# Optimization experiments

Hardware: AMD Instinct MI355X
Metric: run time of the kernel (lower is better)

Reference implementation:

```python
import jax, jax.numpy as jnp
import numpy as np

EMBED_DIM = 1024
NUM_HEADS = 16
HEAD_DIM = EMBED_DIM // NUM_HEADS
B, T = 4, 2048


def setup_inputs() -> dict:
    key = jax.random.key(0)
    ks = jax.random.split(key, 5)
    s = 1.0 / np.sqrt(EMBED_DIM)
    x = jax.random.normal(ks[0], (B, T, EMBED_DIM), dtype=jnp.float32)
    W_qkv = jax.random.uniform(ks[1], (EMBED_DIM, 3 * EMBED_DIM), minval=-s, maxval=s, dtype=jnp.float32)
    b_qkv = jax.random.uniform(ks[2], (3 * EMBED_DIM,), minval=-s, maxval=s, dtype=jnp.float32)
    W_proj = jax.random.uniform(ks[3], (EMBED_DIM, EMBED_DIM), minval=-s, maxval=s, dtype=jnp.float32)
    b_proj = jax.random.uniform(ks[4], (EMBED_DIM,), minval=-s, maxval=s, dtype=jnp.float32)
    return {"x": x, "W_qkv": W_qkv, "b_qkv": b_qkv, "W_proj": W_proj, "b_proj": b_proj}


def reference(x, W_qkv, b_qkv, W_proj, b_proj):
    Bq, Tq, C = x.shape
    H, D = NUM_HEADS, HEAD_DIM
    qkv = x @ W_qkv + b_qkv                      # [B,T,3C]
    qkv = qkv.reshape(Bq, Tq, 3, H, D)
    q = qkv[:, :, 0].transpose(0, 2, 1, 3)       # [B,H,T,D]
    k = qkv[:, :, 1].transpose(0, 2, 1, 3)
    v = qkv[:, :, 2].transpose(0, 2, 1, 3)
    scale = 1.0 / jnp.sqrt(jnp.asarray(D, x.dtype))
    attn = jnp.einsum('bhqd,bhkd->bhqk', q, k) * scale  # [B,H,T,T]
    mask = jnp.tril(jnp.ones((Tq, Tq), dtype=bool))     # causal: keep lower triangle
    attn = jnp.where(mask, attn, jnp.asarray(-jnp.inf, attn.dtype))
    attn = jax.nn.softmax(attn, axis=-1)
    out = jnp.einsum('bhqk,bhkd->bhqd', attn, v)        # [B,H,T,D]
    out = out.transpose(0, 2, 1, 3).reshape(Bq, Tq, C)
    return out @ W_proj + b_proj
```

## Files before the change

### kernel.cpp

```cpp
#include <hip/hip_runtime.h>
#include <stdint.h>

typedef unsigned short ushort_t;
typedef __attribute__((ext_vector_type(4))) unsigned int  u32x4;
typedef __attribute__((ext_vector_type(2))) unsigned int  u32x2;
typedef __attribute__((ext_vector_type(4))) float         f32x4;
typedef __attribute__((ext_vector_type(8))) __bf16        bf16x8;

__device__ __forceinline__ ushort_t f2bf(float f) {
    unsigned int u = __float_as_uint(f);
    u += 0x7fffu + ((u >> 16) & 1u);
    return (ushort_t)(u >> 16);
}
__device__ __forceinline__ unsigned int pack2bf(float a, float b) {
    return (unsigned int)f2bf(a) | ((unsigned int)f2bf(b) << 16);
}
__device__ __forceinline__ f32x4 mfma16(bf16x8 a, bf16x8 b, f32x4 c) {
    return __builtin_amdgcn_mfma_f32_16x16x32_bf16(a, b, c, 0, 0, 0);
}
__device__ __forceinline__ bf16x8 ldfrag(const ushort_t* p) {
    return __builtin_bit_cast(bf16x8, *(const u32x4*)p);
}

typedef __attribute__((address_space(3))) unsigned int lds_u32;
typedef __attribute__((address_space(1))) const unsigned int glb_u32;
__device__ __forceinline__ void async16(const void* g, void* l) {
    __builtin_amdgcn_global_load_lds((glb_u32*)g, (lds_u32*)l, 16, 0, 0);
}

#define QSCALE 0.18033688011112042f

__global__ __launch_bounds__(256) void xcast(const float* __restrict__ X,
                                             ushort_t* __restrict__ Xb) {
    long i = ((long)blockIdx.x * 256 + threadIdx.x) * 8;
    float4 a = *(const float4*)(X + i);
    float4 b = *(const float4*)(X + i + 4);
    u32x4 pk;
    pk.x = pack2bf(a.x, a.y); pk.y = pack2bf(a.z, a.w);
    pk.z = pack2bf(b.x, b.y); pk.w = pack2bf(b.z, b.w);
    *(u32x4*)(Xb + i) = pk;
}

__global__ __launch_bounds__(256) void wt_kernel(const float* __restrict__ W,
                                                 ushort_t* __restrict__ Wt,
                                                 int K, int N) {
    __shared__ float tile[32][33];
    int tx = threadIdx.x, ty = threadIdx.y;
    int n0 = blockIdx.x * 32, k0 = blockIdx.y * 32;
    for (int p = 0; p < 4; ++p)
        tile[ty + 8*p][tx] = W[(long)(k0 + ty + 8*p) * N + n0 + tx];
    __syncthreads();
    for (int p = 0; p < 4; ++p)
        Wt[(long)(n0 + ty + 8*p) * K + k0 + tx] = f2bf(tile[tx][ty + 8*p]);
}

__global__ __launch_bounds__(256) void gemm_qkv(const ushort_t* __restrict__ Xb,
                                                const ushort_t* __restrict__ Wt,
                                                const float* __restrict__ bias,
                                                ushort_t* __restrict__ Qo,
                                                ushort_t* __restrict__ Ko,
                                                ushort_t* __restrict__ Vto) {
    __shared__ __align__(16) ushort_t smem[128 * 136];
    ushort_t* As = smem;
    ushort_t* Bs = smem + 128 * 32;

    const int tid  = threadIdx.x;
    const int g    = blockIdx.x;
    const int grp  = g / 192, rr = g % 192;
    const int m0   = (grp * 8 + (rr & 7)) * 128;
    const int n0   = (rr >> 3) * 128;
    const int lane = tid & 63, w = tid >> 6;
    const int quad = lane >> 4, l16 = lane & 15;
    const int wm = (w >> 1) * 64, wn = (w & 1) * 64;

    const int srow = (lane >> 2);
    const int gch  = (lane & 3) ^ ((lane >> 3) & 3);
    const int rslot = (quad ^ ((l16 >> 1) & 3)) * 8;

    f32x4 acc[4][4] = {};

    for (int k0 = 0; k0 < 1024; k0 += 32) {
        __syncthreads();
        for (int c = 0; c < 2; ++c) {
            int chunk = w * 2 + c;
            int row = chunk * 16 + srow;
            async16(&Xb[(long)(m0 + row) * 1024 + k0 + gch * 8], &As[chunk * 512]);
            async16(&Wt[(long)(n0 + row) * 1024 + k0 + gch * 8], &Bs[chunk * 512]);
        }
        __syncthreads();
        bf16x8 af[4], bfr[4];
        for (int i = 0; i < 4; ++i)
            af[i] = ldfrag(&As[(wm + 16*i + l16) * 32 + rslot]);
        for (int j = 0; j < 4; ++j)
            bfr[j] = ldfrag(&Bs[(wn + 16*j + l16) * 32 + rslot]);
        for (int i = 0; i < 4; ++i)
            for (int j = 0; j < 4; ++j)
                acc[i][j] = mfma16(af[i], bfr[j], acc[i][j]);
    }

    float bj[4];
    for (int j = 0; j < 4; ++j) bj[j] = bias[n0 + wn + 16*j + l16];
    const int bb = m0 >> 11, t0m = m0 & 2047;
    __syncthreads();

    if (n0 < 2048) {
        ushort_t* dst = (n0 < 1024) ? Qo : Ko;
        const float scale = (n0 < 1024) ? QSCALE : 1.0f;
        const int nbase = (n0 < 1024) ? n0 : n0 - 1024;
        for (int i = 0; i < 4; ++i)
            for (int j = 0; j < 4; ++j) {
                int nl = wn + 16*j + l16;
                for (int r = 0; r < 4; ++r) {
                    int ml = wm + 16*i + quad*4 + r;
                    smem[ml * 136 + nl] = f2bf((acc[i][j][r] + bj[j]) * scale);
                }
            }
        __syncthreads();
        for (int c = 0; c < 8; ++c) {
            int chunk = tid + 256 * c;
            int row = chunk >> 4, nc = (chunk & 15) * 8;
            int n = nbase + nc;
            int h = n >> 6, d = n & 63;
            *(u32x4*)&dst[((long)(bb*16 + h) * 2048 + t0m + row) * 64 + d] =
                *(const u32x4*)&smem[row * 136 + nc];
        }
    } else {
        for (int i = 0; i < 4; ++i)
            for (int j = 0; j < 4; ++j) {
                int nl = wn + 16*j + l16;
                for (int r = 0; r < 4; ++r) {
                    int ml = wm + 16*i + quad*4 + r;
                    smem[nl * 136 + ml] = f2bf(acc[i][j][r] + bj[j]);
                }
            }
        __syncthreads();
        for (int c = 0; c < 8; ++c) {
            int chunk = tid + 256 * c;
            int row = chunk >> 4, mc = (chunk & 15) * 8;
            int n = n0 - 2048 + row;
            int h = n >> 6, d = n & 63;
            *(u32x4*)&Vto[((long)(bb*16 + h) * 64 + d) * 2048 + t0m + mc] =
                *(const u32x4*)&smem[row * 136 + mc];
        }
    }
}

__global__ __launch_bounds__(256) void attn_kernel(const ushort_t* __restrict__ Q,
                                                   const ushort_t* __restrict__ K,
                                                   const ushort_t* __restrict__ Vt,
                                                   ushort_t* __restrict__ O) {
    __shared__ __align__(16) ushort_t Ks[64 * 64];
    __shared__ __align__(16) ushort_t Vs[64 * 64];
    __shared__ __align__(16) ushort_t Ps[64 * 72];

    const int tid  = threadIdx.x;
    const int lane = tid & 63, w = tid >> 6, quad = lane >> 4, l16 = lane & 15;
    const int p    = blockIdx.x & 15;
    const int bh   = blockIdx.x >> 4;
    const ushort_t* qptr = Q  + (long)bh * 2048 * 64;
    const ushort_t* kptr = K  + (long)bh * 2048 * 64;
    const ushort_t* vptr = Vt + (long)bh * 64 * 2048;
    const int bb2 = bh >> 4, h = bh & 15;

    const int srow = lane >> 3;
    const int gch  = (lane & 7) ^ (lane >> 3);

    for (int ti = 0; ti < 2; ++ti) {
        const int qt = ti ? (31 - p) : p;
        const int qbase = qt * 64;
        const int nkt = qt + 1;

        __syncthreads();
        for (int c = 0; c < 2; ++c) {
            int chunk = tid + 256 * c;
            int row = chunk >> 3, kc = (chunk & 7) * 8;
            *(u32x4*)&Ps[row * 72 + kc] = *(const u32x4*)&qptr[(long)(qbase + row) * 64 + kc];
        }
        __syncthreads();
        bf16x8 qf[2];
        for (int kk = 0; kk < 2; ++kk)
            qf[kk] = ldfrag(&Ps[(16*w + l16) * 72 + kk*32 + quad*8]);

        f32x4 acc[4] = {};
        float l_run = 0.f;

        for (int kt = 0; kt < nkt; ++kt) {
            const int kbase = kt * 64;
            __syncthreads();
            for (int c = 0; c < 2; ++c) {
                int chunk = w * 2 + c;
                int row = chunk * 8 + srow;
                async16(&kptr[(long)(kbase + row) * 64 + gch * 8], &Ks[chunk * 512]);
                async16(&vptr[(long)row * 2048 + kbase + gch * 8], &Vs[chunk * 512]);
            }
            __syncthreads();

            f32x4 s[4] = {};
            for (int kk = 0; kk < 2; ++kk)
                for (int mt = 0; mt < 4; ++mt) {
                    bf16x8 kf = ldfrag(&Ks[(16*mt + l16) * 64 + ((4*kk + quad) ^ (l16 & 7)) * 8]);
                    s[mt] = mfma16(kf, qf[kk], s[mt]);
                }
            if (kt == nkt - 1) {
                int qv = qbase + 16*w + l16;
                for (int mt = 0; mt < 4; ++mt)
                    for (int r = 0; r < 4; ++r)
                        if (kbase + 16*mt + 4*quad + r > qv)
                            s[mt][r] = -__builtin_inff();
            }
            for (int mt = 0; mt < 4; ++mt) {
                float p0 = exp2f(s[mt][0]), p1 = exp2f(s[mt][1]);
                float p2 = exp2f(s[mt][2]), p3 = exp2f(s[mt][3]);
                l_run += (p0 + p1) + (p2 + p3);
                u32x2 pk;
                pk.x = pack2bf(p0, p1);
                pk.y = pack2bf(p2, p3);
                *(u32x2*)&Ps[(16*w + l16) * 72 + 16*mt + 4*quad] = pk;
            }
            for (int kk = 0; kk < 2; ++kk) {
                bf16x8 pf = ldfrag(&Ps[(16*w + l16) * 72 + kk*32 + quad*8]);
                for (int jd = 0; jd < 4; ++jd) {
                    bf16x8 vf = ldfrag(&Vs[(16*jd + l16) * 64 + ((4*kk + quad) ^ (l16 & 7)) * 8]);
                    acc[jd] = mfma16(pf, vf, acc[jd]);
                }
            }
        }

        l_run += __shfl_xor(l_run, 16, 64);
        l_run += __shfl_xor(l_run, 32, 64);
        float linv[4];
        for (int r = 0; r < 4; ++r)
            linv[r] = 1.0f / __shfl(l_run, (lane & 48) | (4*quad + r), 64);
        for (int jd = 0; jd < 4; ++jd)
            for (int r = 0; r < 4; ++r) {
                int t = qbase + 16*w + 4*quad + r;
                int d = 16*jd + l16;
                O[((long)(bb2*2048 + t)) * 1024 + h*64 + d] = f2bf(acc[jd][r] * linv[r]);
            }
    }
}

__global__ __launch_bounds__(256) void gemm_proj(const ushort_t* __restrict__ A,
                                                 const ushort_t* __restrict__ Wt,
                                                 const float* __restrict__ bias,
                                                 float* __restrict__ Out) {
    __shared__ __align__(16) ushort_t As[128 * 32];
    __shared__ __align__(16) ushort_t Bs[128 * 32];

    const int tid  = threadIdx.x;
    const int g    = blockIdx.x;
    const int grp  = g / 64, rr = g % 64;
    const int m0   = (grp * 8 + (rr & 7)) * 128;
    const int n0   = (rr >> 3) * 128;
    const int lane = tid & 63, w = tid >> 6;
    const int quad = lane >> 4, l16 = lane & 15;
    const int wm = (w >> 1) * 64, wn = (w & 1) * 64;

    const int srow = (lane >> 2);
    const int gch  = (lane & 3) ^ ((lane >> 3) & 3);
    const int rslot = (quad ^ ((l16 >> 1) & 3)) * 8;

    f32x4 acc[4][4] = {};

    for (int k0 = 0; k0 < 1024; k0 += 32) {
        __syncthreads();
        for (int c = 0; c < 2; ++c) {
            int chunk = w * 2 + c;
            int row = chunk * 16 + srow;
            async16(&A [(long)(m0 + row) * 1024 + k0 + gch * 8], &As[chunk * 512]);
            async16(&Wt[(long)(n0 + row) * 1024 + k0 + gch * 8], &Bs[chunk * 512]);
        }
        __syncthreads();
        bf16x8 af[4], bfr[4];
        for (int i = 0; i < 4; ++i)
            af[i] = ldfrag(&As[(wm + 16*i + l16) * 32 + rslot]);
        for (int j = 0; j < 4; ++j)
            bfr[j] = ldfrag(&Bs[(wn + 16*j + l16) * 32 + rslot]);
        for (int i = 0; i < 4; ++i)
            for (int j = 0; j < 4; ++j)
                acc[i][j] = mfma16(af[i], bfr[j], acc[i][j]);
    }

    float bj[4];
    for (int j = 0; j < 4; ++j) bj[j] = bias[n0 + wn + 16*j + l16];
    for (int i = 0; i < 4; ++i)
        for (int j = 0; j < 4; ++j)
            for (int r = 0; r < 4; ++r) {
                int m = m0 + wm + 16*i + quad*4 + r;
                int n = n0 + wn + 16*j + l16;
                Out[(long)m * 1024 + n] = acc[i][j][r] + bj[j];
            }
}

extern "C" void kernel_launch(void* const* d_in, const int* in_sizes, int n_in,
                              void* d_out, int out_size, void* d_ws, size_t ws_size,
                              hipStream_t stream) {
    const float* x     = (const float*)d_in[0];
    const float* Wqkv  = (const float*)d_in[1];
    const float* bqkv  = (const float*)d_in[2];
    const float* Wproj = (const float*)d_in[3];
    const float* bproj = (const float*)d_in[4];
    float* out = (float*)d_out;

    ushort_t* wqkvt  = (ushort_t*)d_ws;
    ushort_t* wprojt = wqkvt  + 3072 * 1024;
    ushort_t* Qb     = wprojt + 1024 * 1024;
    ushort_t* Kb     = Qb  + 8388608;
    ushort_t* Vtb    = Kb  + 8388608;
    ushort_t* XbA2   = Vtb + 8388608;

    xcast<<<4096, 256, 0, stream>>>(x, XbA2);
    wt_kernel<<<dim3(96, 32), dim3(32, 8), 0, stream>>>(Wqkv, wqkvt, 1024, 3072);
    wt_kernel<<<dim3(32, 32), dim3(32, 8), 0, stream>>>(Wproj, wprojt, 1024, 1024);
    gemm_qkv<<<1536, 256, 0, stream>>>(XbA2, wqkvt, bqkv, Qb, Kb, Vtb);
    attn_kernel<<<1024, 256, 0, stream>>>(Qb, Kb, Vtb, XbA2);
    gemm_proj<<<512, 256, 0, stream>>>(XbA2, wprojt, bproj, out);
}
```

Measured before the change: 294.3 us.

## Register-prefetch double-buffered GEMMs and attention with 128-row query tiles

Both GEMMs replace the async global-to-LDS loads with register prefetch of the next K slice and double-buffered LDS, so only one barrier is needed per iteration. The attention kernel moves to 128-row query tiles (two 16-row subtiles per wave), double-buffers K and V through registers, and skips fully masked key tiles per wave. It also uses hardware exp2 and the packed bf16 convert. The intent is to overlap global loads with MFMA work and reuse each K/V tile across more queries, at the cost of more registers and half as many attention blocks.

```diff
diff --git a/kernel.cpp b/kernel.cpp
--- a/kernel.cpp
+++ b/kernel.cpp
@@ -6,6 +6,7 @@
 typedef __attribute__((ext_vector_type(2))) unsigned int  u32x2;
 typedef __attribute__((ext_vector_type(4))) float         f32x4;
 typedef __attribute__((ext_vector_type(8))) __bf16        bf16x8;
+typedef __attribute__((ext_vector_type(2))) __bf16        bf16x2;
 
 __device__ __forceinline__ ushort_t f2bf(float f) {
     unsigned int u = __float_as_uint(f);
@@ -15,17 +16,21 @@
 __device__ __forceinline__ unsigned int pack2bf(float a, float b) {
     return (unsigned int)f2bf(a) | ((unsigned int)f2bf(b) << 16);
 }
+#if __has_builtin(__builtin_amdgcn_cvt_pk_bf16_f32)
+__device__ __forceinline__ unsigned int pack2bf_fast(float a, float b) {
+    bf16x2 v = __builtin_amdgcn_cvt_pk_bf16_f32(a, b);
+    return __builtin_bit_cast(unsigned int, v);
+}
+#else
+__device__ __forceinline__ unsigned int pack2bf_fast(float a, float b) {
+    return pack2bf(a, b);
+}
+#endif
 __device__ __forceinline__ f32x4 mfma16(bf16x8 a, bf16x8 b, f32x4 c) {
     return __builtin_amdgcn_mfma_f32_16x16x32_bf16(a, b, c, 0, 0, 0);
 }
 __device__ __forceinline__ bf16x8 ldfrag(const ushort_t* p) {
     return __builtin_bit_cast(bf16x8, *(const u32x4*)p);
-}
-
-typedef __attribute__((address_space(3))) unsigned int lds_u32;
-typedef __attribute__((address_space(1))) const unsigned int glb_u32;
-__device__ __forceinline__ void async16(const void* g, void* l) {
-    __builtin_amdgcn_global_load_lds((glb_u32*)g, (lds_u32*)l, 16, 0, 0);
 }
 
 #define QSCALE 0.18033688011112042f
@@ -61,8 +66,6 @@
                                                 ushort_t* __restrict__ Ko,
                                                 ushort_t* __restrict__ Vto) {
     __shared__ __align__(16) ushort_t smem[128 * 136];
-    ushort_t* As = smem;
-    ushort_t* Bs = smem + 128 * 32;
 
     const int tid  = threadIdx.x;
     const int g    = blockIdx.x;
@@ -73,21 +76,37 @@
     const int quad = lane >> 4, l16 = lane & 15;
     const int wm = (w >> 1) * 64, wn = (w & 1) * 64;
 
-    const int srow = (lane >> 2);
-    const int gch  = (lane & 3) ^ ((lane >> 3) & 3);
+    const int srow  = tid >> 2;
+    const int slot  = tid & 3;
+    const int oct   = slot ^ ((tid >> 3) & 3);
+    const int wofs  = srow * 32 + slot * 8;
     const int rslot = (quad ^ ((l16 >> 1) & 3)) * 8;
 
+    const ushort_t* Ap = Xb + (long)(m0 + srow) * 1024 + oct * 8;
+    const ushort_t* Bp = Wt + (long)(n0 + srow) * 1024 + oct * 8;
+
     f32x4 acc[4][4] = {};
 
+    u32x4 Ag0 = *(const u32x4*)(Ap);
+    u32x4 Ag1 = *(const u32x4*)(Ap + 65536);
+    u32x4 Bg0 = *(const u32x4*)(Bp);
+    u32x4 Bg1 = *(const u32x4*)(Bp + 65536);
+
     for (int k0 = 0; k0 < 1024; k0 += 32) {
-        __syncthreads();
-        for (int c = 0; c < 2; ++c) {
-            int chunk = w * 2 + c;
-            int row = chunk * 16 + srow;
-            async16(&Xb[(long)(m0 + row) * 1024 + k0 + gch * 8], &As[chunk * 512]);
-            async16(&Wt[(long)(n0 + row) * 1024 + k0 + gch * 8], &Bs[chunk * 512]);
-        }
-        __syncthreads();
+        int kn = (k0 + 32 < 1024) ? k0 + 32 : k0;
+        u32x4 An0 = *(const u32x4*)(Ap + kn);
+        u32x4 An1 = *(const u32x4*)(Ap + kn + 65536);
+        u32x4 Bn0 = *(const u32x4*)(Bp + kn);
+        u32x4 Bn1 = *(const u32x4*)(Bp + kn + 65536);
+
+        ushort_t* As = smem + ((k0 >> 5) & 1) * 4096;
+        ushort_t* Bs = smem + 8192 + ((k0 >> 5) & 1) * 4096;
+        *(u32x4*)&As[wofs]        = Ag0;
+        *(u32x4*)&As[wofs + 2048] = Ag1;
+        *(u32x4*)&Bs[wofs]        = Bg0;
+        *(u32x4*)&Bs[wofs + 2048] = Bg1;
+        __syncthreads();
+
         bf16x8 af[4], bfr[4];
         for (int i = 0; i < 4; ++i)
             af[i] = ldfrag(&As[(wm + 16*i + l16) * 32 + rslot]);
@@ -96,6 +115,8 @@
         for (int i = 0; i < 4; ++i)
             for (int j = 0; j < 4; ++j)
                 acc[i][j] = mfma16(af[i], bfr[j], acc[i][j]);
+
+        Ag0 = An0; Ag1 = An1; Bg0 = Bn0; Bg1 = Bn1;
     }
 
     float bj[4];
@@ -120,8 +141,8 @@
             int chunk = tid + 256 * c;
             int row = chunk >> 4, nc = (chunk & 15) * 8;
             int n = nbase + nc;
-            int h = n >> 6, d = n & 63;
-            *(u32x4*)&dst[((long)(bb*16 + h) * 2048 + t0m + row) * 64 + d] =
+            int hh = n >> 6, d = n & 63;
+            *(u32x4*)&dst[((long)(bb*16 + hh) * 2048 + t0m + row) * 64 + d] =
                 *(const u32x4*)&smem[row * 136 + nc];
         }
     } else {
@@ -138,8 +159,8 @@
             int chunk = tid + 256 * c;
             int row = chunk >> 4, mc = (chunk & 15) * 8;
             int n = n0 - 2048 + row;
-            int h = n >> 6, d = n & 63;
-            *(u32x4*)&Vto[((long)(bb*16 + h) * 64 + d) * 2048 + t0m + mc] =
+            int hh = n >> 6, d = n & 63;
+            *(u32x4*)&Vto[((long)(bb*16 + hh) * 64 + d) * 2048 + t0m + mc] =
                 *(const u32x4*)&smem[row * 136 + mc];
         }
     }
@@ -149,94 +170,122 @@
                                                    const ushort_t* __restrict__ K,
                                                    const ushort_t* __restrict__ Vt,
                                                    ushort_t* __restrict__ O) {
-    __shared__ __align__(16) ushort_t Ks[64 * 64];
-    __shared__ __align__(16) ushort_t Vs[64 * 64];
-    __shared__ __align__(16) ushort_t Ps[64 * 72];
+    __shared__ __align__(16) ushort_t Ks[2][64 * 64];
+    __shared__ __align__(16) ushort_t Vs[2][64 * 64];
+    __shared__ __align__(16) ushort_t Ps[128 * 72];
 
     const int tid  = threadIdx.x;
     const int lane = tid & 63, w = tid >> 6, quad = lane >> 4, l16 = lane & 15;
-    const int p    = blockIdx.x & 15;
-    const int bh   = blockIdx.x >> 4;
+    const int p    = blockIdx.x & 7;
+    const int bh   = blockIdx.x >> 3;
     const ushort_t* qptr = Q  + (long)bh * 2048 * 64;
     const ushort_t* kptr = K  + (long)bh * 2048 * 64;
     const ushort_t* vptr = Vt + (long)bh * 64 * 2048;
     const int bb2 = bh >> 4, h = bh & 15;
 
-    const int srow = lane >> 3;
-    const int gch  = (lane & 7) ^ (lane >> 3);
+    const int srow = tid >> 3;
+    const int slot = tid & 7;
+    const int oct  = slot ^ (srow & 7);
+    const int koff = srow * 64 + oct * 8;
+    const int voff = srow * 2048 + oct * 8;
+    const int wofs = srow * 64 + slot * 8;
 
     for (int ti = 0; ti < 2; ++ti) {
-        const int qt = ti ? (31 - p) : p;
-        const int qbase = qt * 64;
-        const int nkt = qt + 1;
-
-        __syncthreads();
-        for (int c = 0; c < 2; ++c) {
-            int chunk = tid + 256 * c;
-            int row = chunk >> 3, kc = (chunk & 7) * 8;
+        const int qt = ti ? (15 - p) : p;
+        const int qbase = qt * 128;
+        const int nkt = 2 * qt + 2;
+
+        __syncthreads();
+        for (int c = 0; c < 4; ++c) {
+            int flat = tid + 256 * c;
+            int row = flat >> 3, kc = (flat & 7) * 8;
             *(u32x4*)&Ps[row * 72 + kc] = *(const u32x4*)&qptr[(long)(qbase + row) * 64 + kc];
         }
         __syncthreads();
-        bf16x8 qf[2];
-        for (int kk = 0; kk < 2; ++kk)
-            qf[kk] = ldfrag(&Ps[(16*w + l16) * 72 + kk*32 + quad*8]);
-
-        f32x4 acc[4] = {};
-        float l_run = 0.f;
+        bf16x8 qf[2][2];
+        for (int nt = 0; nt < 2; ++nt)
+            for (int kk = 0; kk < 2; ++kk)
+                qf[nt][kk] = ldfrag(&Ps[(32*w + 16*nt + l16) * 72 + kk*32 + quad*8]);
+
+        f32x4 acc[2][4] = {};
+        float l_run[2] = {0.f, 0.f};
+
+        u32x4 Kg0 = *(const u32x4*)(kptr + koff);
+        u32x4 Kg1 = *(const u32x4*)(kptr + koff + 2048);
+        u32x4 Vg0 = *(const u32x4*)(vptr + voff);
+        u32x4 Vg1 = *(const u32x4*)(vptr + voff + 65536);
 
         for (int kt = 0; kt < nkt; ++kt) {
             const int kbase = kt * 64;
+            const int kn = (kt + 1 < nkt) ? kt + 1 : kt;
+            u32x4 Kn0 = *(const u32x4*)(kptr + kn*4096 + koff);
+            u32x4 Kn1 = *(const u32x4*)(kptr + kn*4096 + koff + 2048);
+            u32x4 Vn0 = *(const u32x4*)(vptr + kn*64 + voff);
+            u32x4 Vn1 = *(const u32x4*)(vptr + kn*64 + voff + 65536);
+
+            ushort_t* Kb = Ks[kt & 1];
+            ushort_t* Vb = Vs[kt & 1];
+            *(u32x4*)&Kb[wofs]        = Kg0;
+            *(u32x4*)&Kb[wofs + 2048] = Kg1;
+            *(u32x4*)&Vb[wofs]        = Vg0;
+            *(u32x4*)&Vb[wofs + 2048] = Vg1;
             __syncthreads();
-            for (int c = 0; c < 2; ++c) {
-                int chunk = w * 2 + c;
-                int row = chunk * 8 + srow;
-                async16(&kptr[(long)(kbase + row) * 64 + gch * 8], &Ks[chunk * 512]);
-                async16(&vptr[(long)row * 2048 + kbase + gch * 8], &Vs[chunk * 512]);
-            }
-            __syncthreads();
-
-            f32x4 s[4] = {};
-            for (int kk = 0; kk < 2; ++kk)
-                for (int mt = 0; mt < 4; ++mt) {
-                    bf16x8 kf = ldfrag(&Ks[(16*mt + l16) * 64 + ((4*kk + quad) ^ (l16 & 7)) * 8]);
-                    s[mt] = mfma16(kf, qf[kk], s[mt]);
-                }
-            if (kt == nkt - 1) {
-                int qv = qbase + 16*w + l16;
-                for (int mt = 0; mt < 4; ++mt)
-                    for (int r = 0; r < 4; ++r)
-                        if (kbase + 16*mt + 4*quad + r > qv)
-                            s[mt][r] = -__builtin_inff();
-            }
-            for (int mt = 0; mt < 4; ++mt) {
-                float p0 = exp2f(s[mt][0]), p1 = exp2f(s[mt][1]);
-                float p2 = exp2f(s[mt][2]), p3 = exp2f(s[mt][3]);
-                l_run += (p0 + p1) + (p2 + p3);
-                u32x2 pk;
-                pk.x = pack2bf(p0, p1);
-                pk.y = pack2bf(p2, p3);
-                *(u32x2*)&Ps[(16*w + l16) * 72 + 16*mt + 4*quad] = pk;
-            }
-            for (int kk = 0; kk < 2; ++kk) {
-                bf16x8 pf = ldfrag(&Ps[(16*w + l16) * 72 + kk*32 + quad*8]);
+
+            if (kbase <= qbase + 32*w + 31) {
+                f32x4 s[4][2] = {};
+                for (int kk = 0; kk < 2; ++kk)
+                    for (int mt = 0; mt < 4; ++mt) {
+                        bf16x8 kf = ldfrag(&Kb[(16*mt + l16) * 64 + ((4*kk + quad) ^ (l16 & 7)) * 8]);
+                        for (int nt = 0; nt < 2; ++nt)
+                            s[mt][nt] = mfma16(kf, qf[nt][kk], s[mt][nt]);
+                    }
+                if (kbase + 63 > qbase + 32*w) {
+                    for (int mt = 0; mt < 4; ++mt)
+                        for (int nt = 0; nt < 2; ++nt) {
+                            int qv = qbase + 32*w + 16*nt + l16;
+                            for (int r = 0; r < 4; ++r)
+                                if (kbase + 16*mt + 4*quad + r > qv)
+                                    s[mt][nt][r] = -__builtin_inff();
+                        }
+                }
+                for (int nt = 0; nt < 2; ++nt)
+                    for (int mt = 0; mt < 4; ++mt) {
+                        float p0 = __builtin_amdgcn_exp2f(s[mt][nt][0]);
+                        float p1 = __builtin_amdgcn_exp2f(s[mt][nt][1]);
+                        float p2 = __builtin_amdgcn_exp2f(s[mt][nt][2]);
+                        float p3 = __builtin_amdgcn_exp2f(s[mt][nt][3]);
+                        l_run[nt] += (p0 + p1) + (p2 + p3);
+                        u32x2 pk;
+                        pk.x = pack2bf_fast(p0, p1);
+                        pk.y = pack2bf_fast(p2, p3);
+                        *(u32x2*)&Ps[(32*w + 16*nt + l16) * 72 + 16*mt + 4*quad] = pk;
+                    }
+                for (int kk = 0; kk < 2; ++kk) {
+                    bf16x8 pf0 = ldfrag(&Ps[(32*w + l16) * 72 + kk*32 + quad*8]);
+                    bf16x8 pf1 = ldfrag(&Ps[(32*w + 16 + l16) * 72 + kk*32 + quad*8]);
+                    for (int jd = 0; jd < 4; ++jd) {
+                        bf16x8 vf = ldfrag(&Vb[(16*jd + l16) * 64 + ((4*kk + quad) ^ (l16 & 7)) * 8]);
+                        acc[0][jd] = mfma16(pf0, vf, acc[0][jd]);
+                        acc[1][jd] = mfma16(pf1, vf, acc[1][jd]);
+                    }
+                }
+            }
+            Kg0 = Kn0; Kg1 = Kn1; Vg0 = Vn0; Vg1 = Vn1;
+        }
+
+        for (int i = 0; i < 2; ++i) {
+            float l = l_run[i];
+            l += __shfl_xor(l, 16, 64);
+            l += __shfl_xor(l, 32, 64);
+            for (int r = 0; r < 4; ++r) {
+                float linv = 1.0f / __shfl(l, (lane & 48) | (4*quad + r), 64);
+                int t = qbase + 32*w + 16*i + 4*quad + r;
                 for (int jd = 0; jd < 4; ++jd) {
-                    bf16x8 vf = ldfrag(&Vs[(16*jd + l16) * 64 + ((4*kk + quad) ^ (l16 & 7)) * 8]);
-                    acc[jd] = mfma16(pf, vf, acc[jd]);
-                }
-            }
-        }
-
-        l_run += __shfl_xor(l_run, 16, 64);
-        l_run += __shfl_xor(l_run, 32, 64);
-        float linv[4];
-        for (int r = 0; r < 4; ++r)
-            linv[r] = 1.0f / __shfl(l_run, (lane & 48) | (4*quad + r), 64);
-        for (int jd = 0; jd < 4; ++jd)
-            for (int r = 0; r < 4; ++r) {
-                int t = qbase + 16*w + 4*quad + r;
-                int d = 16*jd + l16;
-                O[((long)(bb2*2048 + t)) * 1024 + h*64 + d] = f2bf(acc[jd][r] * linv[r]);
-            }
+                    int d = 16*jd + l16;
+                    O[((long)(bb2*2048 + t)) * 1024 + h*64 + d] = f2bf(acc[i][jd][r] * linv);
+                }
+            }
+        }
     }
 }
 
@@ -244,8 +293,7 @@
                                                  const ushort_t* __restrict__ Wt,
                                                  const float* __restrict__ bias,
                                                  float* __restrict__ Out) {
-    __shared__ __align__(16) ushort_t As[128 * 32];
-    __shared__ __align__(16) ushort_t Bs[128 * 32];
+    __shared__ __align__(16) ushort_t smem[4 * 4096];
 
     const int tid  = threadIdx.x;
     const int g    = blockIdx.x;
@@ -256,21 +304,37 @@
     const int quad = lane >> 4, l16 = lane & 15;
     const int wm = (w >> 1) * 64, wn = (w & 1) * 64;
 
-    const int srow = (lane >> 2);
-    const int gch  = (lane & 3) ^ ((lane >> 3) & 3);
+    const int srow  = tid >> 2;
+    const int slot  = tid & 3;
+    const int oct   = slot ^ ((tid >> 3) & 3);
+    const int wofs  = srow * 32 + slot * 8;
     const int rslot = (quad ^ ((l16 >> 1) & 3)) * 8;
 
+    const ushort_t* Ap = A  + (long)(m0 + srow) * 1024 + oct * 8;
+    const ushort_t* Bp = Wt + (long)(n0 + srow) * 1024 + oct * 8;
+
     f32x4 acc[4][4] = {};
 
+    u32x4 Ag0 = *(const u32x4*)(Ap);
+    u32x4 Ag1 = *(const u32x4*)(Ap + 65536);
+    u32x4 Bg0 = *(const u32x4*)(Bp);
+    u32x4 Bg1 = *(const u32x4*)(Bp + 65536);
+
     for (int k0 = 0; k0 < 1024; k0 += 32) {
-        __syncthreads();
-        for (int c = 0; c < 2; ++c) {
-            int chunk = w * 2 + c;
-            int row = chunk * 16 + srow;
-            async16(&A [(long)(m0 + row) * 1024 + k0 + gch * 8], &As[chunk * 512]);
-            async16(&Wt[(long)(n0 + row) * 1024 + k0 + gch * 8], &Bs[chunk * 512]);
-        }
-        __syncthreads();
+        int kn = (k0 + 32 < 1024) ? k0 + 32 : k0;
+        u32x4 An0 = *(const u32x4*)(Ap + kn);
+        u32x4 An1 = *(const u32x4*)(Ap + kn + 65536);
+        u32x4 Bn0 = *(const u32x4*)(Bp + kn);
+        u32x4 Bn1 = *(const u32x4*)(Bp + kn + 65536);
+
+        ushort_t* As = smem + ((k0 >> 5) & 1) * 4096;
+        ushort_t* Bs = smem + 8192 + ((k0 >> 5) & 1) * 4096;
+        *(u32x4*)&As[wofs]        = Ag0;
+        *(u32x4*)&As[wofs + 2048] = Ag1;
+        *(u32x4*)&Bs[wofs]        = Bg0;
+        *(u32x4*)&Bs[wofs + 2048] = Bg1;
+        __syncthreads();
+
         bf16x8 af[4], bfr[4];
         for (int i = 0; i < 4; ++i)
             af[i] = ldfrag(&As[(wm + 16*i + l16) * 32 + rslot]);
@@ -279,6 +343,8 @@
         for (int i = 0; i < 4; ++i)
             for (int j = 0; j < 4; ++j)
                 acc[i][j] = mfma16(af[i], bfr[j], acc[i][j]);
+
+        Ag0 = An0; Ag1 = An1; Bg0 = Bn0; Bg1 = Bn1;
     }
 
     float bj[4];
@@ -313,6 +379,6 @@
     wt_kernel<<<dim3(96, 32), dim3(32, 8), 0, stream>>>(Wqkv, wqkvt, 1024, 3072);
     wt_kernel<<<dim3(32, 32), dim3(32, 8), 0, stream>>>(Wproj, wprojt, 1024, 1024);
     gemm_qkv<<<1536, 256, 0, stream>>>(XbA2, wqkvt, bqkv, Qb, Kb, Vtb);
-    attn_kernel<<<1024, 256, 0, stream>>>(Qb, Kb, Vtb, XbA2);
+    attn_kernel<<<512, 256, 0, stream>>>(Qb, Kb, Vtb, XbA2);
     gemm_proj<<<512, 256, 0, stream>>>(XbA2, wprojt, bproj, out);
 }
```

New measurement: 258.7 us. -12.1%, faster.
